# Optimization experiments

Hardware: AMD Instinct MI355X
Metric: run time of the kernel (lower is better)

The kernel has to match this reference:

```python
import jax, jax.numpy as jnp
import numpy as np

DIM = 384
HEADS = 6
EPS = 1e-5
SCALE = DIM ** -0.5  # note: original uses full dim, not head_dim


def _dwconv_bn(x, w, stride, g, b, m, v):
    # x: [B, C, H, W], w: [C, 1, 3, 3] depthwise
    y = jax.lax.conv_general_dilated(
        x, w, window_strides=(stride, stride), padding=((1, 1), (1, 1)),
        dimension_numbers=('NCHW', 'OIHW', 'NCHW'), feature_group_count=DIM)
    # BatchNorm2d inference form
    inv = jax.lax.rsqrt(v + EPS)
    y = (y - m[None, :, None, None]) * (inv * g)[None, :, None, None] + b[None, :, None, None]
    # b c h w -> b (h w) c
    B, C, H, W = y.shape
    return y.reshape(B, C, H * W).transpose(0, 2, 1)


def setup_inputs() -> dict:
    key = jax.random.key(0)
    ks = jax.random.split(key, 24)
    d = {}
    d['x'] = jax.random.normal(ks[0], (8, 3136, DIM), jnp.float32)
    d['h'] = 56
    d['w'] = 56
    i = 1
    for nm in ('q', 'k', 'v'):
        d[f'conv_{nm}'] = jax.random.normal(ks[i], (DIM, 1, 3, 3), jnp.float32) * 0.1; i += 1
        d[f'bn{nm}_s'] = jnp.ones((DIM,), jnp.float32)
        d[f'bn{nm}_b'] = jnp.zeros((DIM,), jnp.float32)
        d[f'bn{nm}_m'] = jax.random.normal(ks[i], (DIM,), jnp.float32) * 0.1; i += 1
        d[f'bn{nm}_v'] = jax.random.uniform(ks[i], (DIM,), jnp.float32) + 0.5; i += 1
    s = DIM ** -0.5
    d['wq'] = jax.random.normal(ks[i], (DIM, DIM), jnp.float32) * s; i += 1
    d['wk'] = jax.random.normal(ks[i], (DIM, DIM), jnp.float32) * s; i += 1
    d['wv'] = jax.random.normal(ks[i], (DIM, DIM), jnp.float32) * s; i += 1
    d['w_last'] = jax.random.normal(ks[i], (DIM, DIM), jnp.float32) * s; i += 1
    d['b_last'] = jnp.zeros((DIM,), jnp.float32)
    return d


def reference(x, h, w, conv_q, bnq_s, bnq_b, bnq_m, bnq_v,
              conv_k, bnk_s, bnk_b, bnk_m, bnk_v,
              conv_v, bnv_s, bnv_b, bnv_m, bnv_v,
              wq, wk, wv, w_last, b_last):
    B, T, C = x.shape
    xim = x.transpose(0, 2, 1).reshape(B, C, h, w)  # b (h w) c -> b c h w
    q = _dwconv_bn(xim, conv_q, 1, bnq_s, bnq_b, bnq_m, bnq_v)  # [B, h*w, C]
    k = _dwconv_bn(xim, conv_k, 2, bnk_s, bnk_b, bnk_m, bnk_v)  # [B, hw/4, C]
    v = _dwconv_bn(xim, conv_v, 2, bnv_s, bnv_b, bnv_m, bnv_v)
    # linear projections (torch Linear: y = x @ W.T), split heads
    def heads(t, W):
        y = jnp.einsum('btc,oc->bto', t, W)
        Bt, Tt, _ = y.shape
        return y.reshape(Bt, Tt, HEADS, C // HEADS).transpose(0, 2, 1, 3)
    qh, kh, vh = heads(q, wq), heads(k, wk), heads(v, wv)
    attn = jax.nn.softmax(jnp.einsum('bhld,bhtd->bhlt', qh, kh) * SCALE, axis=-1)
    o = jnp.einsum('bhlt,bhtd->bhld', attn, vh)  # [B, H, L, d]
    o = o.transpose(0, 2, 1, 3).reshape(B, T, C)
    return jnp.einsum('btc,oc->bto', o, w_last) + b_last
```

## Files before the change

### kernel.cpp

```cpp
#include <hip/hip_runtime.h>
#include <hip/hip_bf16.h>

typedef __bf16 bf16;
typedef __attribute__((ext_vector_type(8))) __bf16 bf16x8;
typedef __attribute__((ext_vector_type(4))) __bf16 bf16x4;
typedef __attribute__((ext_vector_type(2))) __bf16 bf16x2;
typedef __attribute__((ext_vector_type(16))) float floatx16;
typedef unsigned int u32;

#define MFMA32(a, b, c) __builtin_amdgcn_mfma_f32_32x32x16_bf16((a), (b), (c), 0, 0, 0)

#define DIM 384
#define T1 3136
#define T2 784
#define T2P 832
#define B_ 8
#define EPSV 1e-5f

__device__ __forceinline__ void gload_lds16(const bf16* g, bf16* l) {
  __builtin_amdgcn_global_load_lds(
      (const __attribute__((address_space(1))) void*)g,
      (__attribute__((address_space(3))) void*)l, 16, 0, 0);
}

__device__ __forceinline__ u32 pk2(float a, float b) {
  bf16x2 t = (bf16x2){(bf16)a, (bf16)b};
  return *reinterpret_cast<u32*>(&t);
}

__global__ void conv_fused_kernel(const float* __restrict__ x,
    const float* __restrict__ wqc, const float* __restrict__ gq, const float* __restrict__ bq,
    const float* __restrict__ mq, const float* __restrict__ vq,
    const float* __restrict__ wkc, const float* __restrict__ gk, const float* __restrict__ bk,
    const float* __restrict__ mk, const float* __restrict__ vk,
    const float* __restrict__ wvc, const float* __restrict__ gv, const float* __restrict__ bv,
    const float* __restrict__ mv, const float* __restrict__ vvv,
    bf16* __restrict__ qout, bf16* __restrict__ kout, bf16* __restrict__ vout,
    const float* __restrict__ w0, const float* __restrict__ w1,
    const float* __restrict__ w2, const float* __restrict__ w3,
    bf16* __restrict__ d0, bf16* __restrict__ d1,
    bf16* __restrict__ d2, bf16* __restrict__ d3) {
  int blk = blockIdx.x;
  int c = threadIdx.x;
  int gid = blk * DIM + c;
  if (gid < 147456) {
    d0[gid] = (bf16)w0[gid]; d1[gid] = (bf16)w1[gid];
    d2[gid] = (bf16)w2[gid]; d3[gid] = (bf16)w3[gid];
  }
  int xg = blk % 14;
  int y = (blk / 14) % 56;
  int b = blk / (14 * 56);
  int x0 = xg * 4;
  const float* xb = x + (size_t)b * T1 * DIM;
  float in[3][6];
#pragma unroll
  for (int r = 0; r < 3; ++r) {
    int yy = y + r - 1;
#pragma unroll
    for (int cc = 0; cc < 6; ++cc) {
      int xc = x0 + cc - 1;
      in[r][cc] = (yy >= 0 && yy < 56 && xc >= 0 && xc < 56)
                      ? xb[(yy * 56 + xc) * DIM + c] : 0.f;
    }
  }
  {
    float wr[9];
#pragma unroll
    for (int i = 0; i < 9; ++i) wr[i] = wqc[c * 9 + i];
    float a = rsqrtf(vq[c] + EPSV) * gq[c];
    float bia = bq[c] - mq[c] * a;
#pragma unroll
    for (int p = 0; p < 4; ++p) {
      float s = 0.f;
#pragma unroll
      for (int r = 0; r < 3; ++r)
#pragma unroll
        for (int dx = 0; dx < 3; ++dx) s += in[r][p + dx] * wr[r * 3 + dx];
      qout[((size_t)b * T1 + y * 56 + x0 + p) * DIM + c] = (bf16)(s * a + bia);
    }
  }
  if ((y & 1) == 0) {
    int y2 = y >> 1;
    float wk9[9], wv9[9];
#pragma unroll
    for (int i = 0; i < 9; ++i) { wk9[i] = wkc[c * 9 + i]; wv9[i] = wvc[c * 9 + i]; }
    float ak = rsqrtf(vk[c] + EPSV) * gk[c];
    float av = rsqrtf(vvv[c] + EPSV) * gv[c];
    float bik = bk[c] - mk[c] * ak;
    float biv = bv[c] - mv[c] * av;
#pragma unroll
    for (int p2 = 0; p2 < 2; ++p2) {
      float sk = 0.f, sv = 0.f;
#pragma unroll
      for (int r = 0; r < 3; ++r)
#pragma unroll
        for (int dx = 0; dx < 3; ++dx) {
          float xv = in[r][2 * p2 + dx];
          sk += xv * wk9[r * 3 + dx];
          sv += xv * wv9[r * 3 + dx];
        }
      size_t o = ((size_t)b * T2 + y2 * 28 + (x0 >> 1) + p2) * DIM + c;
      kout[o] = (bf16)(sk * ak + bik);
      vout[o] = (bf16)(sv * av + biv);
    }
  }
}

#define BK64 64
#define ABUF (256 * BK64)
#define BBUF (128 * BK64)
__device__ __forceinline__
void gemm512_body(const bf16* A, const bf16* Bw, void* out, const float* bias,
                  int mode, float scale, int m0, int n0, int Mrows,
                  bf16* Al, bf16* Bl) {
  int tid = threadIdx.x;
  int w = tid >> 6, lane = tid & 63;
  int wm = w >> 1, wn = w & 1;
  int l32 = lane & 31, hi = lane >> 5;

  int arow = lane >> 3;
  int achk = (lane & 7) ^ arow;
  const bf16* ag0 = &A[(size_t)(m0 + w * 32 + arow) * DIM + achk * 8];
  const bf16* bg0 = &Bw[(size_t)(n0 + w * 16 + arow) * DIM + achk * 8];

  floatx16 acc[2][2];
  acc[0][0] = (floatx16)0.f; acc[0][1] = (floatx16)0.f;
  acc[1][0] = (floatx16)0.f; acc[1][1] = (floatx16)0.f;

  auto STAGE = [&](int s) {
    int bi = s & 1;
    int k = s * BK64;
    bf16* ad = Al + bi * ABUF + (w * 32) * BK64;
    bf16* bd = Bl + bi * BBUF + (w * 16) * BK64;
    gload_lds16(ag0 + k, ad);
    gload_lds16(ag0 + (size_t)8 * DIM + k, ad + 8 * BK64);
    gload_lds16(ag0 + (size_t)16 * DIM + k, ad + 16 * BK64);
    gload_lds16(ag0 + (size_t)24 * DIM + k, ad + 24 * BK64);
    gload_lds16(bg0 + k, bd);
    gload_lds16(bg0 + (size_t)8 * DIM + k, bd + 8 * BK64);
  };

  STAGE(0);
  const int NS = DIM / BK64;
#pragma unroll
  for (int s = 0; s < NS; ++s) {
    const int cb = s & 1;
    if (s + 1 < NS) {
      STAGE(s + 1);
      asm volatile("s_waitcnt vmcnt(6)" ::: "memory");
    } else {
      asm volatile("s_waitcnt vmcnt(0)" ::: "memory");
    }
    __builtin_amdgcn_s_barrier();
    const bf16* Ac = Al + cb * ABUF;
    const bf16* Bc = Bl + cb * BBUF;
#pragma unroll
    for (int ksp = 0; ksp < 2; ++ksp) {
      bf16x8 af[2][2], bfr[2][2];
#pragma unroll
      for (int kh = 0; kh < 2; ++kh) {
        int ks = ksp * 2 + kh;
        int ch = ((ks * 2 + hi) ^ (l32 & 7)) * 8;
#pragma unroll
        for (int mt = 0; mt < 2; ++mt)
          af[mt][kh] = *(const bf16x8*)&Ac[(wm * 64 + mt * 32 + l32) * BK64 + ch];
#pragma unroll
        for (int nt = 0; nt < 2; ++nt)
          bfr[nt][kh] = *(const bf16x8*)&Bc[(wn * 64 + nt * 32 + l32) * BK64 + ch];
      }
#pragma unroll
      for (int kh = 0; kh < 2; ++kh)
#pragma unroll
        for (int mt = 0; mt < 2; ++mt)
#pragma unroll
          for (int nt = 0; nt < 2; ++nt)
            acc[mt][nt] = MFMA32(af[mt][kh], bfr[nt][kh], acc[mt][nt]);
    }
    asm volatile("s_waitcnt lgkmcnt(0)" ::: "memory");
    __builtin_amdgcn_s_barrier();
  }
#pragma unroll
  for (int mt = 0; mt < 2; ++mt) {
#pragma unroll
    for (int nt = 0; nt < 2; ++nt) {
      int col = n0 + wn * 64 + nt * 32 + l32;
#pragma unroll
      for (int r = 0; r < 16; ++r) {
        int row = m0 + wm * 64 + mt * 32 + (r & 3) + 8 * (r >> 2) + 4 * hi;
        float v = acc[mt][nt][r];
        if (mode == 3) {
          ((float*)out)[(size_t)row * DIM + col] = v + bias[col];
        } else if (mode == 2) {
          if (row < Mrows) {
            int b = row / T2;
            int t = row - b * T2;
            ((bf16*)out)[((size_t)b * DIM + col) * T2P + t] = (bf16)v;
          }
        } else if (mode == 0) {
          if (row < Mrows) ((bf16*)out)[(size_t)row * DIM + col] = (bf16)v;
        } else {
          ((bf16*)out)[(size_t)row * DIM + col] = (bf16)(v * scale);
        }
      }
    }
  }
}

__global__ __launch_bounds__(512, 2)
void qkv_gemm_kernel(const bf16* q_act, const bf16* k_act, const bf16* v_act,
                     const bf16* wqb, const bf16* wkb, const bf16* wvb,
                     bf16* Qp, bf16* Kp, bf16* Vtp, float qscale) {
  __shared__ bf16 Al[2 * ABUF];
  __shared__ bf16 Bl[2 * BBUF];
  int bx = blockIdx.x;
  int t = (bx & 7) * 56 + (bx >> 3);
  if (t >= 444) return;
  const bf16 *A, *Bw; void* out; int mode, ti, M; float scale = 1.f;
  if (t < 294)      { A = q_act; Bw = wqb; out = Qp;  mode = 1; ti = t;       M = T1 * B_; scale = qscale; }
  else if (t < 369) { A = k_act; Bw = wkb; out = Kp;  mode = 0; ti = t - 294; M = T2 * B_; }
  else              { A = v_act; Bw = wvb; out = Vtp; mode = 2; ti = t - 369; M = T2 * B_; }
  gemm512_body(A, Bw, out, nullptr, mode, scale, (ti / 3) * 256, (ti % 3) * 128, M, Al, Bl);
}

__global__ __launch_bounds__(512, 2)
void last_gemm_kernel(const bf16* A, const bf16* Bw, float* out, const float* bias) {
  __shared__ bf16 Al[2 * ABUF];
  __shared__ bf16 Bl[2 * BBUF];
  int bx = blockIdx.x;
  int t = (bx & 7) * 37 + (bx >> 3);
  if (t >= 294) return;
  gemm512_body(A, Bw, out, bias, 3, 1.f, (t / 3) * 256, (t % 3) * 128, T1 * B_, Al, Bl);
}

__global__ __launch_bounds__(256, 4)
void attn_kernel(const bf16* __restrict__ Qp, const bf16* __restrict__ Kp,
                 const bf16* __restrict__ Vt, bf16* __restrict__ Ob) {
  __shared__ bf16 Kl[64 * 64];
  __shared__ bf16 Vl[64 * 64];
  int bx = blockIdx.x;
  int xcd = bx & 7, j = bx >> 3;
  int g = xcd + 8 * (j / 25);
  int qblk = j % 25;
  int h = g % 6;
  int b = g / 6;
  int tid = threadIdx.x, w = tid >> 6, lane = tid & 63;
  int l32 = lane & 31, hi = lane >> 5;
  int q0w = qblk * 128 + w * 32;

  bf16x8 qf[4];
  {
    int qi = q0w + l32;
    qi = qi < T1 ? qi : T1 - 1;
    const bf16* qp = &Qp[((size_t)b * T1 + qi) * DIM + h * 64];
#pragma unroll
    for (int kk = 0; kk < 4; ++kk) qf[kk] = *(const bf16x8*)&qp[kk * 16 + hi * 8];
  }
  floatx16 oacc[2];
  oacc[0] = (floatx16)0.f;
  oacc[1] = (floatx16)0.f;
  float lsum = 0.f;

  int rsub = lane >> 3;
  int chnk = (lane & 7) ^ rsub;
  const bf16* kg0 = &Kp[((size_t)b * T2 + w * 16 + rsub) * DIM + h * 64 + chnk * 8];
  const bf16* kg1 = kg0 + (size_t)8 * DIM;
  const bf16* vg0 = &Vt[((size_t)b * DIM + h * 64 + w * 16 + rsub) * T2P + chnk * 8];
  const bf16* vg1 = vg0 + (size_t)8 * T2P;
  bf16* kl0 = &Kl[(w * 16) * 64];
  bf16* kl1 = &Kl[(w * 16 + 8) * 64];
  bf16* vl0 = &Vl[(w * 16) * 64];
  bf16* vl1 = &Vl[(w * 16 + 8) * 64];

  int key = lane & 7;

  for (int it = 0; it < 12; ++it) {
    __syncthreads();
    gload_lds16(kg0, kl0);
    gload_lds16(kg1, kl1);
    gload_lds16(vg0, vl0);
    gload_lds16(vg1, vl1);
    __syncthreads();
#pragma unroll
    for (int tt = 0; tt < 2; ++tt) {
      floatx16 s = (floatx16)0.f;
#pragma unroll
      for (int kk = 0; kk < 4; ++kk) {
        bf16x8 kf = *(const bf16x8*)&Kl[(tt * 32 + l32) * 64 + ((kk * 2 + hi) ^ key) * 8];
        s = MFMA32(kf, qf[kk], s);
      }
      float e[16];
#pragma unroll
      for (int r = 0; r < 16; ++r) {
        e[r] = __builtin_amdgcn_exp2f(s[r]);
        lsum += e[r];
      }
#pragma unroll
      for (int kkl = 0; kkl < 2; ++kkl) {
        int r0 = kkl * 8;
        u32 pA = pk2(e[r0 + 0], e[r0 + 1]);
        u32 pB = pk2(e[r0 + 2], e[r0 + 3]);
        u32 pC = pk2(e[r0 + 4], e[r0 + 5]);
        u32 pD = pk2(e[r0 + 6], e[r0 + 7]);
        u32 sA = __shfl_xor(pA, 32);
        u32 sB = __shfl_xor(pB, 32);
        u32 sC = __shfl_xor(pC, 32);
        u32 sD = __shfl_xor(pD, 32);
        union { u32 u[4]; bf16x8 v; } pf;
        pf.u[0] = hi ? sC : pA;
        pf.u[1] = hi ? sD : pB;
        pf.u[2] = hi ? pC : sA;
        pf.u[3] = hi ? pD : sB;
        int kk = tt * 2 + kkl;
#pragma unroll
        for (int dt = 0; dt < 2; ++dt) {
          bf16x8 vf = *(const bf16x8*)&Vl[(dt * 32 + l32) * 64 + ((kk * 2 + hi) ^ key) * 8];
          oacc[dt] = MFMA32(vf, pf.v, oacc[dt]);
        }
      }
    }
    kg0 += (size_t)64 * DIM; kg1 += (size_t)64 * DIM;
    vg0 += 64; vg1 += 64;
  }
  {
    int tq = 768 + l32;
    tq = tq < T2 ? tq : T2 - 1;
    const bf16* kp2 = &Kp[((size_t)b * T2 + tq) * DIM + h * 64];
    floatx16 s = (floatx16)0.f;
#pragma unroll
    for (int kk = 0; kk < 4; ++kk) {
      bf16x8 kf = *(const bf16x8*)&kp2[kk * 16 + hi * 8];
      s = MFMA32(kf, qf[kk], s);
    }
    float e[8];
#pragma unroll
    for (int r = 0; r < 8; ++r) {
      e[r] = __builtin_amdgcn_exp2f(s[r]);
      lsum += e[r];
    }
    u32 pA = pk2(e[0], e[1]);
    u32 pB = pk2(e[2], e[3]);
    u32 pC = pk2(e[4], e[5]);
    u32 pD = pk2(e[6], e[7]);
    u32 sA = __shfl_xor(pA, 32);
    u32 sB = __shfl_xor(pB, 32);
    u32 sC = __shfl_xor(pC, 32);
    u32 sD = __shfl_xor(pD, 32);
    union { u32 u[4]; bf16x8 v; } pf;
    pf.u[0] = hi ? sC : pA;
    pf.u[1] = hi ? sD : pB;
    pf.u[2] = hi ? pC : sA;
    pf.u[3] = hi ? pD : sB;
#pragma unroll
    for (int dt = 0; dt < 2; ++dt) {
      const bf16* vp2 = &Vt[((size_t)b * DIM + h * 64 + dt * 32 + l32) * T2P + 768 + hi * 8];
      bf16x8 vf = *(const bf16x8*)vp2;
      oacc[dt] = MFMA32(vf, pf.v, oacc[dt]);
    }
  }
  lsum += __shfl_xor(lsum, 32);
  float inv = 1.f / lsum;
  int qg = q0w + l32;
  if (qg < T1) {
    bf16* op = &Ob[((size_t)b * T1 + qg) * DIM + h * 64];
#pragma unroll
    for (int dt = 0; dt < 2; ++dt) {
#pragma unroll
      for (int gr = 0; gr < 4; ++gr) {
        bf16x4 ov = (bf16x4){(bf16)(oacc[dt][gr * 4 + 0] * inv),
                             (bf16)(oacc[dt][gr * 4 + 1] * inv),
                             (bf16)(oacc[dt][gr * 4 + 2] * inv),
                             (bf16)(oacc[dt][gr * 4 + 3] * inv)};
        *(bf16x4*)&op[dt * 32 + gr * 8 + hi * 4] = ov;
      }
    }
  }
}

extern "C" void kernel_launch(void* const* d_in, const int* in_sizes, int n_in,
                              void* d_out, int out_size, void* d_ws, size_t ws_size,
                              hipStream_t stream) {
  (void)in_sizes; (void)n_in; (void)out_size; (void)ws_size;
  const float* x      = (const float*)d_in[0];
  const float* conv_q = (const float*)d_in[3];
  const float* bnq_s  = (const float*)d_in[4];
  const float* bnq_b  = (const float*)d_in[5];
  const float* bnq_m  = (const float*)d_in[6];
  const float* bnq_v  = (const float*)d_in[7];
  const float* conv_k = (const float*)d_in[8];
  const float* bnk_s  = (const float*)d_in[9];
  const float* bnk_b  = (const float*)d_in[10];
  const float* bnk_m  = (const float*)d_in[11];
  const float* bnk_v  = (const float*)d_in[12];
  const float* conv_v = (const float*)d_in[13];
  const float* bnv_s  = (const float*)d_in[14];
  const float* bnv_b  = (const float*)d_in[15];
  const float* bnv_m  = (const float*)d_in[16];
  const float* bnv_v  = (const float*)d_in[17];
  const float* wq     = (const float*)d_in[18];
  const float* wk     = (const float*)d_in[19];
  const float* wv     = (const float*)d_in[20];
  const float* wl     = (const float*)d_in[21];
  const float* b_last = (const float*)d_in[22];

  char* ws = (char*)d_ws;
  bf16* q_act = (bf16*)(ws + 0);
  bf16* k_act = (bf16*)(ws + 19267584);
  bf16* v_act = (bf16*)(ws + 24084480);
  bf16* Qp    = (bf16*)(ws + 28901376);
  bf16* Kp    = (bf16*)(ws + 48168960);
  bf16* Vtp   = (bf16*)(ws + 52985856);
  bf16* wqb   = (bf16*)(ws + 58097664);
  bf16* wkb   = wqb + 147456;
  bf16* wvb   = wkb + 147456;
  bf16* wlb   = wvb + 147456;

  const float QSCALE = 0.05103103630798288f * 1.4426950408889634f;

  conv_fused_kernel<<<B_ * 56 * 14, DIM, 0, stream>>>(
      x,
      conv_q, bnq_s, bnq_b, bnq_m, bnq_v,
      conv_k, bnk_s, bnk_b, bnk_m, bnk_v,
      conv_v, bnv_s, bnv_b, bnv_m, bnv_v,
      q_act, k_act, v_act,
      wq, wk, wv, wl, wqb, wkb, wvb, wlb);

  qkv_gemm_kernel<<<448, 512, 0, stream>>>(q_act, k_act, v_act, wqb, wkb, wvb,
                                           Qp, Kp, Vtp, QSCALE);

  attn_kernel<<<25 * 6 * B_, 256, 0, stream>>>(Qp, Kp, Vtp, q_act);

  last_gemm_kernel<<<296, 512, 0, stream>>>(q_act, wlb, (float*)d_out, b_last);
}
```

Baseline: 269.8 us.

## Replace 512-thread GEMM tiles with single-wave 64x64 tiles and triple buffering

Rewrites the shared GEMM body so that each block is a single 64-lane wave computing a 64x64 output tile, with a 16-wide K step and a three-stage LDS ring that holds no barriers. The QKV and output-projection launches grow to thousands of small blocks. The aim is to remove block-wide barriers and to balance load across CUs better. In exchange, each block reuses far less data (64x64 tiles with K=16 per stage) and issues many more small global-to-LDS loads, and row bounds checks are dropped on the assumption that the row counts divide evenly by 64.

```diff
diff --git a/kernel.cpp b/kernel.cpp
--- a/kernel.cpp
+++ b/kernel.cpp
@@ -106,98 +106,83 @@
   }
 }
 
-#define BK64 64
-#define ABUF (256 * BK64)
-#define BBUF (128 * BK64)
+#define WBK 16
+#define WBUF (64 * WBK)
 __device__ __forceinline__
-void gemm512_body(const bf16* A, const bf16* Bw, void* out, const float* bias,
-                  int mode, float scale, int m0, int n0, int Mrows,
-                  bf16* Al, bf16* Bl) {
-  int tid = threadIdx.x;
-  int w = tid >> 6, lane = tid & 63;
-  int wm = w >> 1, wn = w & 1;
+void wgemm_body(const bf16* A, const bf16* Bw, void* out, const float* bias,
+                int mode, float scale, int m0, int n0, bf16* Ab, bf16* Bb) {
+  int lane = threadIdx.x;
   int l32 = lane & 31, hi = lane >> 5;
 
-  int arow = lane >> 3;
-  int achk = (lane & 7) ^ arow;
-  const bf16* ag0 = &A[(size_t)(m0 + w * 32 + arow) * DIM + achk * 8];
-  const bf16* bg0 = &Bw[(size_t)(n0 + w * 16 + arow) * DIM + achk * 8];
+  const bf16* ag = &A[(size_t)(m0 + (lane >> 1)) * DIM + (lane & 1) * 8];
+  const bf16* bg = &Bw[(size_t)(n0 + (lane >> 1)) * DIM + (lane & 1) * 8];
 
   floatx16 acc[2][2];
   acc[0][0] = (floatx16)0.f; acc[0][1] = (floatx16)0.f;
   acc[1][0] = (floatx16)0.f; acc[1][1] = (floatx16)0.f;
 
-  auto STAGE = [&](int s) {
-    int bi = s & 1;
-    int k = s * BK64;
-    bf16* ad = Al + bi * ABUF + (w * 32) * BK64;
-    bf16* bd = Bl + bi * BBUF + (w * 16) * BK64;
-    gload_lds16(ag0 + k, ad);
-    gload_lds16(ag0 + (size_t)8 * DIM + k, ad + 8 * BK64);
-    gload_lds16(ag0 + (size_t)16 * DIM + k, ad + 16 * BK64);
-    gload_lds16(ag0 + (size_t)24 * DIM + k, ad + 24 * BK64);
-    gload_lds16(bg0 + k, bd);
-    gload_lds16(bg0 + (size_t)8 * DIM + k, bd + 8 * BK64);
-  };
+  const int NS = DIM / WBK;
+
+#define STAGE(s) {                                            \
+    bf16* ad = Ab + ((s) % 3) * WBUF;                         \
+    bf16* bd = Bb + ((s) % 3) * WBUF;                         \
+    int kk = (s) * WBK;                                       \
+    gload_lds16(ag + kk, ad);                                 \
+    gload_lds16(ag + (size_t)32 * DIM + kk, ad + 32 * WBK);   \
+    gload_lds16(bg + kk, bd);                                 \
+    gload_lds16(bg + (size_t)32 * DIM + kk, bd + 32 * WBK);   \
+  }
+
+  bf16x8 fa[2][2], fb[2][2];
+#define LOADF(s) {                                                        \
+    const bf16* As = Ab + ((s) % 3) * WBUF;                               \
+    const bf16* Bs = Bb + ((s) % 3) * WBUF;                               \
+    fa[(s) & 1][0] = *(const bf16x8*)&As[(l32) * WBK + hi * 8];           \
+    fa[(s) & 1][1] = *(const bf16x8*)&As[(32 + l32) * WBK + hi * 8];      \
+    fb[(s) & 1][0] = *(const bf16x8*)&Bs[(l32) * WBK + hi * 8];           \
+    fb[(s) & 1][1] = *(const bf16x8*)&Bs[(32 + l32) * WBK + hi * 8];      \
+  }
 
   STAGE(0);
-  const int NS = DIM / BK64;
+  STAGE(1);
+  asm volatile("s_waitcnt vmcnt(4)" ::: "memory");
+  LOADF(0);
 #pragma unroll
   for (int s = 0; s < NS; ++s) {
-    const int cb = s & 1;
-    if (s + 1 < NS) {
-      STAGE(s + 1);
-      asm volatile("s_waitcnt vmcnt(6)" ::: "memory");
-    } else {
+    if (s + 2 < NS) {
+      STAGE(s + 2);
+      asm volatile("s_waitcnt vmcnt(4)" ::: "memory");
+      LOADF(s + 1);
+    } else if (s + 1 < NS) {
       asm volatile("s_waitcnt vmcnt(0)" ::: "memory");
-    }
-    __builtin_amdgcn_s_barrier();
-    const bf16* Ac = Al + cb * ABUF;
-    const bf16* Bc = Bl + cb * BBUF;
-#pragma unroll
-    for (int ksp = 0; ksp < 2; ++ksp) {
-      bf16x8 af[2][2], bfr[2][2];
-#pragma unroll
-      for (int kh = 0; kh < 2; ++kh) {
-        int ks = ksp * 2 + kh;
-        int ch = ((ks * 2 + hi) ^ (l32 & 7)) * 8;
-#pragma unroll
-        for (int mt = 0; mt < 2; ++mt)
-          af[mt][kh] = *(const bf16x8*)&Ac[(wm * 64 + mt * 32 + l32) * BK64 + ch];
-#pragma unroll
-        for (int nt = 0; nt < 2; ++nt)
-          bfr[nt][kh] = *(const bf16x8*)&Bc[(wn * 64 + nt * 32 + l32) * BK64 + ch];
-      }
-#pragma unroll
-      for (int kh = 0; kh < 2; ++kh)
-#pragma unroll
-        for (int mt = 0; mt < 2; ++mt)
-#pragma unroll
-          for (int nt = 0; nt < 2; ++nt)
-            acc[mt][nt] = MFMA32(af[mt][kh], bfr[nt][kh], acc[mt][nt]);
-    }
-    asm volatile("s_waitcnt lgkmcnt(0)" ::: "memory");
-    __builtin_amdgcn_s_barrier();
-  }
+      LOADF(s + 1);
+    }
+    const int p = s & 1;
+#pragma unroll
+    for (int mt = 0; mt < 2; ++mt)
+#pragma unroll
+      for (int nt = 0; nt < 2; ++nt)
+        acc[mt][nt] = MFMA32(fa[p][mt], fb[p][nt], acc[mt][nt]);
+  }
+#undef STAGE
+#undef LOADF
 #pragma unroll
   for (int mt = 0; mt < 2; ++mt) {
 #pragma unroll
     for (int nt = 0; nt < 2; ++nt) {
-      int col = n0 + wn * 64 + nt * 32 + l32;
+      int col = n0 + nt * 32 + l32;
 #pragma unroll
       for (int r = 0; r < 16; ++r) {
-        int row = m0 + wm * 64 + mt * 32 + (r & 3) + 8 * (r >> 2) + 4 * hi;
+        int row = m0 + mt * 32 + (r & 3) + 8 * (r >> 2) + 4 * hi;
         float v = acc[mt][nt][r];
         if (mode == 3) {
           ((float*)out)[(size_t)row * DIM + col] = v + bias[col];
         } else if (mode == 2) {
-          if (row < Mrows) {
-            int b = row / T2;
-            int t = row - b * T2;
-            ((bf16*)out)[((size_t)b * DIM + col) * T2P + t] = (bf16)v;
-          }
+          int b = row / T2;
+          int t = row - b * T2;
+          ((bf16*)out)[((size_t)b * DIM + col) * T2P + t] = (bf16)v;
         } else if (mode == 0) {
-          if (row < Mrows) ((bf16*)out)[(size_t)row * DIM + col] = (bf16)v;
+          ((bf16*)out)[(size_t)row * DIM + col] = (bf16)v;
         } else {
           ((bf16*)out)[(size_t)row * DIM + col] = (bf16)(v * scale);
         }
@@ -206,30 +191,28 @@
   }
 }
 
-__global__ __launch_bounds__(512, 2)
+__global__ __launch_bounds__(64, 3)
 void qkv_gemm_kernel(const bf16* q_act, const bf16* k_act, const bf16* v_act,
                      const bf16* wqb, const bf16* wkb, const bf16* wvb,
                      bf16* Qp, bf16* Kp, bf16* Vtp, float qscale) {
-  __shared__ bf16 Al[2 * ABUF];
-  __shared__ bf16 Bl[2 * BBUF];
+  __shared__ bf16 Ab[3 * WBUF];
+  __shared__ bf16 Bb[3 * WBUF];
   int bx = blockIdx.x;
-  int t = (bx & 7) * 56 + (bx >> 3);
-  if (t >= 444) return;
-  const bf16 *A, *Bw; void* out; int mode, ti, M; float scale = 1.f;
-  if (t < 294)      { A = q_act; Bw = wqb; out = Qp;  mode = 1; ti = t;       M = T1 * B_; scale = qscale; }
-  else if (t < 369) { A = k_act; Bw = wkb; out = Kp;  mode = 0; ti = t - 294; M = T2 * B_; }
-  else              { A = v_act; Bw = wvb; out = Vtp; mode = 2; ti = t - 369; M = T2 * B_; }
-  gemm512_body(A, Bw, out, nullptr, mode, scale, (ti / 3) * 256, (ti % 3) * 128, M, Al, Bl);
-}
-
-__global__ __launch_bounds__(512, 2)
+  int t = (bx & 7) * 441 + (bx >> 3);
+  const bf16 *A, *Bw; void* out; int mode, ti; float scale = 1.f;
+  if (t < 2352)      { A = q_act; Bw = wqb; out = Qp;  mode = 1; ti = t;        scale = qscale; }
+  else if (t < 2940) { A = k_act; Bw = wkb; out = Kp;  mode = 0; ti = t - 2352; }
+  else               { A = v_act; Bw = wvb; out = Vtp; mode = 2; ti = t - 2940; }
+  wgemm_body(A, Bw, out, nullptr, mode, scale, (ti / 6) * 64, (ti % 6) * 64, Ab, Bb);
+}
+
+__global__ __launch_bounds__(64, 3)
 void last_gemm_kernel(const bf16* A, const bf16* Bw, float* out, const float* bias) {
-  __shared__ bf16 Al[2 * ABUF];
-  __shared__ bf16 Bl[2 * BBUF];
+  __shared__ bf16 Ab[3 * WBUF];
+  __shared__ bf16 Bb[3 * WBUF];
   int bx = blockIdx.x;
-  int t = (bx & 7) * 37 + (bx >> 3);
-  if (t >= 294) return;
-  gemm512_body(A, Bw, out, bias, 3, 1.f, (t / 3) * 256, (t % 3) * 128, T1 * B_, Al, Bl);
+  int t = (bx & 7) * 294 + (bx >> 3);
+  wgemm_body(A, Bw, out, bias, 3, 1.f, (t / 6) * 64, (t % 6) * 64, Ab, Bb);
 }
 
 __global__ __launch_bounds__(256, 4)
@@ -424,10 +407,10 @@
       q_act, k_act, v_act,
       wq, wk, wv, wl, wqb, wkb, wvb, wlb);
 
-  qkv_gemm_kernel<<<448, 512, 0, stream>>>(q_act, k_act, v_act, wqb, wkb, wvb,
+  qkv_gemm_kernel<<<3528, 64, 0, stream>>>(q_act, k_act, v_act, wqb, wkb, wvb,
                                            Qp, Kp, Vtp, QSCALE);
 
   attn_kernel<<<25 * 6 * B_, 256, 0, stream>>>(Qp, Kp, Vtp, q_act);
 
-  last_gemm_kernel<<<296, 512, 0, stream>>>(q_act, wlb, (float*)d_out, b_last);
-}
+  last_gemm_kernel<<<2352, 64, 0, stream>>>(q_act, wlb, (float*)d_out, b_last);
+}
```

Measured after the change: 303.9 us. +12.6%, slower.
